# Performance work log

Hardware: AMD Instinct MI355X
Metric: run time of the kernel (lower is better)

## Reference

```python
import jax, jax.numpy as jnp
import numpy as np

B, T, D = 2, 2048, 2048
H, K, Hd = 16, 8, 128
EPS = 1e-6
THETA = 1e6


def _rms_norm(x, w):
    # x: [..., Hd]
    return x * jax.lax.rsqrt(jnp.mean(x * x, axis=-1, keepdims=True) + EPS) * w


def _rope(x, sin, cos):
    # x: [B, T, Hh, Hd]; sin/cos: [T, Hd//2]
    s = sin[None, :, None, :]
    c = cos[None, :, None, :]
    x1 = x[..., 0::2]
    x2 = x[..., 1::2]
    # NOTE: source concatenates halves (non-interleaved output), replicate exactly
    return jnp.concatenate([x1 * c - x2 * s, x1 * s + x2 * c], axis=-1)


def setup_inputs() -> dict:
    key = jax.random.key(0)
    ks = jax.random.split(key, 5)
    scale = 0.02
    x = jax.random.normal(ks[0], (B, T, D), dtype=jnp.float32)
    Wq = jax.random.normal(ks[1], (D, H * Hd), dtype=jnp.float32) * scale
    Wk = jax.random.normal(ks[2], (D, K * Hd), dtype=jnp.float32) * scale
    Wv = jax.random.normal(ks[3], (D, K * Hd), dtype=jnp.float32) * scale
    Wo = jax.random.normal(ks[4], (H * Hd, D), dtype=jnp.float32) * scale
    qn_w = jnp.ones((Hd,), dtype=jnp.float32)
    kn_w = jnp.ones((Hd,), dtype=jnp.float32)
    # RotaryEmbedding: inv_freq = theta**(-arange(0,Hd,2)/Hd); freqs = outer(t, inv_freq)
    inv_freq = 1.0 / (THETA ** (jnp.arange(0, Hd, 2, dtype=jnp.float32) / Hd))
    freqs = jnp.arange(T, dtype=jnp.float32)[:, None] * inv_freq[None, :]
    return {"x": x, "Wq": Wq, "Wk": Wk, "Wv": Wv, "Wo": Wo,
            "qn_w": qn_w, "kn_w": kn_w,
            "sin": jnp.sin(freqs), "cos": jnp.cos(freqs)}


def reference(x, Wq, Wk, Wv, Wo, qn_w, kn_w, sin, cos):
    Bx, Tx, _ = x.shape
    q = (x @ Wq).reshape(Bx, Tx, H, Hd)
    k = (x @ Wk).reshape(Bx, Tx, K, Hd)
    v = (x @ Wv).reshape(Bx, Tx, K, Hd)
    q = _rope(_rms_norm(q, qn_w), sin, cos)
    k = _rope(_rms_norm(k, kn_w), sin, cos)
    q = q.transpose(0, 2, 1, 3)  # [B,H,T,Hd]
    k = k.transpose(0, 2, 1, 3)  # [B,K,T,Hd]
    v = v.transpose(0, 2, 1, 3)
    if K != 1 and K != H:
        rep = H // K
        k = jnp.repeat(k, rep, axis=1)  # repeat_interleave on head dim
        v = jnp.repeat(v, rep, axis=1)
    att = jnp.einsum('bhqd,bhkd->bhqk', q.astype(jnp.float32),
                     k.astype(jnp.float32)) / np.sqrt(Hd).astype(np.float32)
    causal = jnp.tril(jnp.ones((Tx, Tx), dtype=bool))
    att = jnp.where(causal[None, None], att, -jnp.inf)
    att = jax.nn.softmax(att, axis=-1)
    out = jnp.einsum('bhqk,bhkd->bhqd', att, v.astype(jnp.float32))
    out = out.astype(q.dtype).transpose(0, 2, 1, 3).reshape(Bx, Tx, H * Hd)
    return out @ Wo
```

## Files before the change

kernel.cpp:

```cpp
#include <hip/hip_runtime.h>
#include <stdint.h>


#define B_ 2
#define T_ 2048
#define D_ 2048
#define H_ 16
#define KH_ 8
#define HD_ 128
#define M_ (B_*T_)
#define NQKV_ 4096
#define QK_SCALE_LOG2E 0.1275174337f

typedef unsigned short u16;
typedef unsigned int   u32;
typedef __attribute__((ext_vector_type(8)))  __bf16 bf16x8_t;
typedef __attribute__((ext_vector_type(4)))  float  f32x4_t;
typedef __attribute__((ext_vector_type(16))) float  f32x16_t;
typedef __attribute__((ext_vector_type(4)))  u32    u32x4_t;

__device__ __forceinline__ u16 f2bf(float f) {
    u32 x = __float_as_uint(f);
    return (u16)((x + 0x7fffu + ((x >> 16) & 1u)) >> 16);
}
__device__ __forceinline__ u32 pack2(u16 a, u16 b) { return (u32)a | ((u32)b << 16); }

__device__ __forceinline__ void gload16(const void* g, void* l) {
    __builtin_amdgcn_global_load_lds(
        (__attribute__((address_space(1))) const void*)(unsigned long long)g,
        (__attribute__((address_space(3))) void*)(u32)(unsigned long long)l,
        16, 0, 0);
}

__global__ void cast_x_kernel(const float* __restrict__ in, u16* __restrict__ out) {
    int i = (blockIdx.x * 256 + threadIdx.x) * 4;
    float4 v = *(const float4*)(in + i);
    u32 lo = pack2(f2bf(v.x), f2bf(v.y));
    u32 hi = pack2(f2bf(v.z), f2bf(v.w));
    *(uint2*)(out + i) = make_uint2(lo, hi);
}

__global__ void tcast_kernel(const float* __restrict__ in, u16* __restrict__ out,
                             int ncols) {
    __shared__ u16 tile[64][65];
    int k0 = blockIdx.x * 64;
    int n0 = blockIdx.y * 64;
    int tid = threadIdx.x;
#pragma unroll
    for (int i = 0; i < 8; ++i) {
        int idx = tid + i * 256;
        int r = idx >> 5, c2 = idx & 31;
        float2 v = *(const float2*)(in + (size_t)(k0 + r) * ncols + n0 + 2 * c2);
        tile[r][2 * c2]     = f2bf(v.x);
        tile[r][2 * c2 + 1] = f2bf(v.y);
    }
    __syncthreads();
#pragma unroll
    for (int i = 0; i < 8; ++i) {
        int idx = tid + i * 256;
        int rn = idx >> 5, c2 = idx & 31;
        *(u32*)(out + (size_t)(n0 + rn) * 2048 + k0 + 2 * c2) =
            pack2(tile[2 * c2][rn], tile[2 * c2 + 1][rn]);
    }
}

#define NKT 32

__global__ void __launch_bounds__(512, 2)
gemm8p_kernel(const u16* __restrict__ A, const u16* __restrict__ Bt,
              float* __restrict__ C, int N) {
    __shared__ u16 As[2][256 * 64];
    __shared__ u16 Bs[2][256 * 64];
    const int tid  = threadIdx.x;
    const int lane = tid & 63;
    const int w    = tid >> 6;
    const int wm   = w >> 2;
    const int wn   = w & 3;
    const int m0 = blockIdx.x * 256;
    const int n0 = blockIdx.y * 256;
    const int fr = lane & 15;
    const int kg = lane >> 4;

    const u16* Ag = A  + (size_t)m0 * 2048;
    const u16* Bg = Bt + (size_t)n0 * 2048;

#define STG(gbase, lbase, h, kt_)                                              \
    do {                                                                       \
        int _k0 = (kt_) * 64;                                                  \
        _Pragma("unroll")                                                      \
        for (int _i = 0; _i < 2; ++_i) {                                       \
            int _r  = _i * 64 + w * 8 + (lane >> 3);                           \
            int _sl = (lane & 7) ^ (_r & 7);                                   \
            gload16((gbase) + (size_t)((h) * 128 + _r) * 2048 + _k0 + _sl * 8, \
                    (lbase) + (h) * 8192 + (_i * 512 + w * 64) * 8);           \
        }                                                                      \
    } while (0)

    bf16x8_t afr[4][2];
    bf16x8_t bfr[2][2][2];
    f32x4_t  acc[8][4];
#pragma unroll
    for (int i = 0; i < 8; ++i)
#pragma unroll
        for (int j = 0; j < 4; ++j)
#pragma unroll
            for (int e = 0; e < 4; ++e) acc[i][j][e] = 0.0f;

#define RDA(qm)                                                                \
    _Pragma("unroll")                                                          \
    for (int _mf = 0; _mf < 4; ++_mf)                                          \
        _Pragma("unroll")                                                      \
        for (int _ks = 0; _ks < 2; ++_ks) {                                    \
            int _row  = wm * 128 + ((qm) * 4 + _mf) * 16 + fr;                 \
            int _phys = (_ks * 4 + kg) ^ (_row & 7);                           \
            afr[_mf][_ks] = *(const bf16x8_t*)(Asc + _row * 64 + _phys * 8);   \
        }
#define RDB(qn)                                                                \
    _Pragma("unroll")                                                          \
    for (int _nf = 0; _nf < 2; ++_nf)                                          \
        _Pragma("unroll")                                                      \
        for (int _ks = 0; _ks < 2; ++_ks) {                                    \
            int _row  = wn * 64 + ((qn) * 2 + _nf) * 16 + fr;                  \
            int _phys = (_ks * 4 + kg) ^ (_row & 7);                           \
            bfr[qn][_nf][_ks] = *(const bf16x8_t*)(Bsc + _row * 64 + _phys * 8);\
        }
#define MM(qm, qn)                                                             \
    _Pragma("unroll")                                                          \
    for (int _mf = 0; _mf < 4; ++_mf)                                          \
        _Pragma("unroll")                                                      \
        for (int _nf = 0; _nf < 2; ++_nf)                                      \
            _Pragma("unroll")                                                  \
            for (int _ks = 0; _ks < 2; ++_ks)                                  \
                acc[(qm) * 4 + _mf][(qn) * 2 + _nf] =                          \
                    __builtin_amdgcn_mfma_f32_16x16x32_bf16(                   \
                        afr[_mf][_ks], bfr[qn][_nf][_ks],                      \
                        acc[(qm) * 4 + _mf][(qn) * 2 + _nf], 0, 0, 0);

#define SBAR __builtin_amdgcn_sched_barrier(0)
#define PH_MID                                                                 \
    SBAR; __builtin_amdgcn_s_barrier();                                        \
    asm volatile("s_waitcnt lgkmcnt(0)" ::: "memory"); SBAR;                   \
    __builtin_amdgcn_s_setprio(1)
#define PH_END                                                                 \
    __builtin_amdgcn_s_setprio(0); SBAR;                                       \
    __builtin_amdgcn_s_barrier(); SBAR

    STG(Ag, &As[0][0], 0, 0);
    STG(Ag, &As[0][0], 1, 0);
    STG(Bg, &Bs[0][0], 0, 0);
    STG(Bg, &Bs[0][0], 1, 0);
    STG(Bg, &Bs[1][0], 0, 1);
    STG(Bg, &Bs[1][0], 1, 1);
    asm volatile("s_waitcnt vmcnt(4)" ::: "memory");
    SBAR;
    __builtin_amdgcn_s_barrier();
    SBAR;

    for (int kt = 0; kt < NKT; ++kt) {
        const int cur = kt & 1;
        const u16* Asc = &As[cur][0];
        const u16* Bsc = &Bs[cur][0];
        u16* Aso = &As[cur ^ 1][0];
        u16* Bsw = &Bs[cur][0];
        RDA(0); RDB(0);
        if (kt + 1 < NKT) STG(Ag, Aso, 0, kt + 1);
        PH_MID; MM(0, 0); PH_END;
        RDB(1);
        if (kt + 1 < NKT) STG(Ag, Aso, 1, kt + 1);
        PH_MID; MM(0, 1); PH_END;
        RDA(1);
        if (kt + 2 < NKT) STG(Bg, Bsw, 0, kt + 2);
        PH_MID; MM(1, 0); PH_END;
        if (kt + 2 < NKT) STG(Bg, Bsw, 1, kt + 2);
        SBAR; __builtin_amdgcn_s_barrier(); SBAR;
        __builtin_amdgcn_s_setprio(1);
        MM(1, 1);
        __builtin_amdgcn_s_setprio(0); SBAR;
        if (kt < NKT - 2) asm volatile("s_waitcnt vmcnt(4)" ::: "memory");
        else              asm volatile("s_waitcnt vmcnt(0)" ::: "memory");
        SBAR;
        __builtin_amdgcn_s_barrier();
        SBAR;
    }
#undef STG
#undef RDA
#undef RDB
#undef MM
#undef PH_MID
#undef PH_END

#pragma unroll
    for (int mf = 0; mf < 8; ++mf)
#pragma unroll
        for (int nf = 0; nf < 4; ++nf) {
            int colx  = n0 + wn * 64 + nf * 16 + fr;
            int rbase = m0 + wm * 128 + mf * 16 + kg * 4;
#pragma unroll
            for (int j = 0; j < 4; ++j)
                C[(size_t)(rbase + j) * N + colx] = acc[mf][nf][j];
        }
}

__global__ void __launch_bounds__(256)
normrope_kernel(const float* __restrict__ Cqkv,
                const float* __restrict__ qw, const float* __restrict__ kw,
                const float* __restrict__ sinT, const float* __restrict__ cosT,
                u16* __restrict__ qbf, u16* __restrict__ kbf, u16* __restrict__ vbf) {
    int lane = threadIdx.x & 63;
    int w    = threadIdx.x >> 6;
    int rid  = blockIdx.x * 4 + w;
    int m   = rid >> 5;
    int sub = rid & 31;
    int b = m >> 11, t = m & (T_ - 1);

    if (sub >= 24) {
        int kh = sub - 24;
        float2 x = *(const float2*)(Cqkv + (size_t)m * NQKV_ + 3072 + kh * HD_ + 2 * lane);
        *(u32*)(vbf + ((size_t)(b * KH_ + kh) * T_ + t) * HD_ + 2 * lane) =
            pack2(f2bf(x.x), f2bf(x.y));
        return;
    }
    bool isq = sub < 16;
    int  hh  = isq ? sub : sub - 16;
    int  colbase = isq ? hh * HD_ : 2048 + hh * HD_;
    float2 x = *(const float2*)(Cqkv + (size_t)m * NQKV_ + colbase + 2 * lane);
    float ss = x.x * x.x + x.y * x.y;
#pragma unroll
    for (int sh = 1; sh < 64; sh <<= 1) ss += __shfl_xor(ss, sh, 64);
    float scale = rsqrtf(ss * (1.0f / 128.0f) + 1e-6f);
    const float* wp = isq ? qw : kw;
    float2 wv = *(const float2*)(wp + 2 * lane);
    float y1 = x.x * scale * wv.x;
    float y2 = x.y * scale * wv.y;
    float c = cosT[t * 64 + lane], s = sinT[t * 64 + lane];
    float oa = y1 * c - y2 * s;
    float ob = y1 * s + y2 * c;
    if (isq) { oa *= QK_SCALE_LOG2E; ob *= QK_SCALE_LOG2E; }
    u16* outp = isq ? (qbf + ((size_t)(b * H_  + hh) * T_ + t) * HD_)
                    : (kbf + ((size_t)(b * KH_ + hh) * T_ + t) * HD_);
    outp[lane]      = f2bf(oa);
    outp[64 + lane] = f2bf(ob);
}

__global__ void vtrans_kernel(const u16* __restrict__ in, u16* __restrict__ out) {
    __shared__ u16 tile[64][65];
    int t0 = blockIdx.x * 64;
    int d0 = blockIdx.y * 64;
    size_t bi = (size_t)blockIdx.z * T_ * HD_;
    size_t bo = (size_t)blockIdx.z * HD_ * T_;
    int tid = threadIdx.x;
#pragma unroll
    for (int i = 0; i < 8; ++i) {
        int idx = tid + i * 256;
        int r = idx >> 5, c2 = idx & 31;
        u32 v = *(const u32*)(in + bi + (size_t)(t0 + r) * HD_ + d0 + 2 * c2);
        tile[r][2 * c2]     = (u16)(v & 0xffffu);
        tile[r][2 * c2 + 1] = (u16)(v >> 16);
    }
    __syncthreads();
#pragma unroll
    for (int i = 0; i < 8; ++i) {
        int idx = tid + i * 256;
        int rd = idx >> 5, c2 = idx & 31;
        *(u32*)(out + bo + (size_t)(d0 + rd) * T_ + t0 + 2 * c2) =
            pack2(tile[2 * c2][rd], tile[2 * c2 + 1][rd]);
    }
}

__global__ void __launch_bounds__(256, 2)
attn_kernel(const u16* __restrict__ qg, const u16* __restrict__ kgl,
            const u16* __restrict__ vtg, u16* __restrict__ attout) {
    __shared__ u16 Kt[2][64 * 128];
    __shared__ u16 Vt[2][128 * 64];

    const int tid = threadIdx.x, lane = tid & 63, w = tid >> 6;
    const int qb = (int)gridDim.x - 1 - (int)blockIdx.x;
    const int h = blockIdx.y, b = blockIdx.z;
    const int kh = h >> 1;
    const int q0 = qb * 128;
    const int col = lane & 31;
    const int hi  = lane >> 5;
    const int l7  = lane & 7;
    const int l15 = lane & 15;
    const int qw0 = q0 + w * 32;
    const int qlane = qw0 + col;

    const u16* qbase = qg  + ((size_t)(b * H_  + h ) * T_) * HD_;
    const u16* kbase = kgl + ((size_t)(b * KH_ + kh) * T_) * HD_;
    const u16* vbase = vtg + ((size_t)(b * KH_ + kh) * HD_) * T_;

    bf16x8_t qf[8];
#pragma unroll
    for (int s = 0; s < 8; ++s)
        qf[s] = *(const bf16x8_t*)(qbase + (size_t)qlane * HD_ + s * 16 + hi * 8);

    const int krl = lane >> 4, kcl = lane & 15;
    const int vrl = lane >> 3, vcl = lane & 7;

    f32x16_t o[4];
#pragma unroll
    for (int dt = 0; dt < 4; ++dt)
#pragma unroll
        for (int r = 0; r < 16; ++r) o[dt][r] = 0.0f;
    float mrow = -1e30f, lrow = 0.0f;

    const int nt = 2 * (qb + 1);

#define STAGE(buf, tt)                                                          \
    do {                                                                        \
        int kv0s = (tt) * 64;                                                   \
        _Pragma("unroll")                                                       \
        for (int cc = 0; cc < 4; ++cc) {                                        \
            int c = w * 4 + cc;                                                 \
            int r = c * 4 + krl;                                                \
            gload16(kbase + (size_t)(kv0s + r) * HD_ + (kcl ^ (r & 15)) * 8,    \
                    &Kt[buf][c * 512]);                                         \
            int rv = c * 8 + vrl;                                               \
            gload16(vbase + (size_t)rv * T_ + kv0s + (vcl ^ (rv & 7)) * 8,      \
                    &Vt[buf][c * 512]);                                         \
        }                                                                       \
    } while (0)

    STAGE(0, 0);
    __syncthreads();

    for (int t = 0; t < nt; ++t) {
        const int cur = t & 1;
        const int kv0 = t * 64;
        if (t + 1 < nt) STAGE(cur ^ 1, t + 1);

        if (kv0 <= qw0 + 31) {
            f32x16_t s0, s1;
#pragma unroll
            for (int r = 0; r < 16; ++r) { s0[r] = 0.0f; s1[r] = 0.0f; }
            __builtin_amdgcn_s_setprio(1);
#pragma unroll
            for (int ss = 0; ss < 8; ++ss) {
                bf16x8_t kf0 = *(const bf16x8_t*)
                    (&Kt[cur][col * 128 + (((2 * ss + hi) ^ l15) * 8)]);
                s0 = __builtin_amdgcn_mfma_f32_32x32x16_bf16(kf0, qf[ss], s0, 0, 0, 0);
                bf16x8_t kf1 = *(const bf16x8_t*)
                    (&Kt[cur][(32 + col) * 128 + (((2 * ss + hi) ^ l15) * 8)]);
                s1 = __builtin_amdgcn_mfma_f32_32x32x16_bf16(kf1, qf[ss], s1, 0, 0, 0);
            }
            __builtin_amdgcn_s_setprio(0);
            if (kv0 + 63 > qw0) {
#pragma unroll
                for (int r = 0; r < 16; ++r) {
                    int cr = (r & 3) + 8 * (r >> 2) + 4 * hi;
                    if (kv0 + cr      > qlane) s0[r] = -1e30f;
                    if (kv0 + 32 + cr > qlane) s1[r] = -1e30f;
                }
            }
            float tmax = s0[0];
#pragma unroll
            for (int r = 1; r < 16; ++r) tmax = fmaxf(tmax, s0[r]);
#pragma unroll
            for (int r = 0; r < 16; ++r) tmax = fmaxf(tmax, s1[r]);
            tmax = fmaxf(tmax, __shfl_xor(tmax, 32, 64));
            float mnew = fmaxf(mrow, tmax);
            float corr = exp2f(mrow - mnew);
            mrow = mnew;
            float ps = 0.0f;
#pragma unroll
            for (int r = 0; r < 16; ++r) {
                s0[r] = exp2f(s0[r] - mrow); ps += s0[r];
                s1[r] = exp2f(s1[r] - mrow); ps += s1[r];
            }
            lrow = lrow * corr + ps;
#pragma unroll
            for (int dt = 0; dt < 4; ++dt)
#pragma unroll
                for (int r = 0; r < 16; ++r) o[dt][r] *= corr;
            u32 pd0[8], pd1[8], po0[8], po1[8];
#pragma unroll
            for (int i = 0; i < 8; ++i) {
                pd0[i] = pack2(f2bf(s0[2 * i]), f2bf(s0[2 * i + 1]));
                pd1[i] = pack2(f2bf(s1[2 * i]), f2bf(s1[2 * i + 1]));
                po0[i] = __shfl_xor(pd0[i], 32, 64);
                po1[i] = __shfl_xor(pd1[i], 32, 64);
            }
            bf16x8_t pf[4];
#pragma unroll
            for (int ks = 0; ks < 4; ++ks) {
                const u32* pd = (ks < 2) ? pd0 : pd1;
                const u32* po = (ks < 2) ? po0 : po1;
                int base = (ks & 1) * 4;
                union { u32 u[4]; bf16x8_t v; } f;
                f.u[0] = hi ? po[base + 2] : pd[base + 0];
                f.u[1] = hi ? po[base + 3] : pd[base + 1];
                f.u[2] = hi ? pd[base + 2] : po[base + 0];
                f.u[3] = hi ? pd[base + 3] : po[base + 1];
                pf[ks] = f.v;
            }
            __builtin_amdgcn_s_setprio(1);
#pragma unroll
            for (int dt = 0; dt < 4; ++dt) {
                int dl = dt * 32 + col;
#pragma unroll
                for (int ks = 0; ks < 4; ++ks) {
                    bf16x8_t vf = *(const bf16x8_t*)
                        (&Vt[cur][dl * 64 + (((2 * ks + hi) ^ l7) * 8)]);
                    o[dt] = __builtin_amdgcn_mfma_f32_32x32x16_bf16(vf, pf[ks], o[dt], 0, 0, 0);
                }
            }
            __builtin_amdgcn_s_setprio(0);
        }
        __syncthreads();
    }
#undef STAGE

    float ltot = lrow + __shfl_xor(lrow, 32, 64);
    float inv  = 1.0f / ltot;
    u16* Tr = &Kt[0][0] + w * 4096;
#pragma unroll
    for (int dt = 0; dt < 4; ++dt)
#pragma unroll
        for (int g = 0; g < 4; ++g) {
            int slot = ((dt << 2) | g) ^ (col & 7);
            u32 lo  = pack2(f2bf(o[dt][4 * g + 0] * inv), f2bf(o[dt][4 * g + 1] * inv));
            u32 hi2 = pack2(f2bf(o[dt][4 * g + 2] * inv), f2bf(o[dt][4 * g + 3] * inv));
            *(uint2*)(Tr + col * 128 + slot * 8 + 4 * hi) = make_uint2(lo, hi2);
        }
    size_t rowbase = (size_t)(b * T_ + qw0);
#pragma unroll
    for (int p = 0; p < 8; ++p) {
        int ql   = p * 4 + (lane >> 4);
        int slot = lane & 15;
        int dl   = (slot ^ (ql & 7)) * 8;
        u32x4_t v = *(const u32x4_t*)(Tr + ql * 128 + slot * 8);
        *(u32x4_t*)(attout + (rowbase + ql) * 2048 + h * HD_ + dl) = v;
    }
}

extern "C" void kernel_launch(void* const* d_in, const int* in_sizes, int n_in,
                              void* d_out, int out_size, void* d_ws, size_t ws_size,
                              hipStream_t stream) {
    const float* x    = (const float*)d_in[0];
    const float* Wq   = (const float*)d_in[1];
    const float* Wk   = (const float*)d_in[2];
    const float* Wv   = (const float*)d_in[3];
    const float* Wo   = (const float*)d_in[4];
    const float* qw   = (const float*)d_in[5];
    const float* kw   = (const float*)d_in[6];
    const float* sinT = (const float*)d_in[7];
    const float* cosT = (const float*)d_in[8];
    float* out = (float*)d_out;

    u16*  x_bf   = (u16*)d_ws;
    u16*  wqkv_t = x_bf   + (size_t)M_ * D_;
    u16*  wo_t   = wqkv_t + (size_t)4096 * 2048;
    float* c_qkv = (float*)(wo_t + (size_t)2048 * 2048);
    u16*  q_bf   = (u16*)(c_qkv + (size_t)M_ * NQKV_);
    u16*  k_bf   = q_bf + (size_t)B_ * H_  * T_ * HD_;
    u16*  v_bf   = k_bf + (size_t)B_ * KH_ * T_ * HD_;
    u16*  v_t    = v_bf + (size_t)B_ * KH_ * T_ * HD_;
    u16*  att_bf = v_t  + (size_t)B_ * KH_ * T_ * HD_;

    cast_x_kernel<<<(M_ * D_) / 1024, 256, 0, stream>>>(x, x_bf);
    tcast_kernel<<<dim3(32, 32), 256, 0, stream>>>(Wq, wqkv_t, 2048);
    tcast_kernel<<<dim3(32, 16), 256, 0, stream>>>(Wk, wqkv_t + (size_t)2048 * 2048, 1024);
    tcast_kernel<<<dim3(32, 16), 256, 0, stream>>>(Wv, wqkv_t + (size_t)3072 * 2048, 1024);
    tcast_kernel<<<dim3(32, 32), 256, 0, stream>>>(Wo, wo_t, 2048);

    gemm8p_kernel<<<dim3(16, 16), 512, 0, stream>>>(x_bf, wqkv_t, c_qkv, 4096);
    normrope_kernel<<<(M_ * 32) / 4, 256, 0, stream>>>(c_qkv, qw, kw, sinT, cosT,
                                                       q_bf, k_bf, v_bf);
    vtrans_kernel<<<dim3(32, 2, 16), 256, 0, stream>>>(v_bf, v_t);
    attn_kernel<<<dim3(16, 16, 2), 256, 0, stream>>>(q_bf, k_bf, v_t, att_bf);
    gemm8p_kernel<<<dim3(16, 8), 512, 0, stream>>>(att_bf, wo_t, out, 2048);
}
```

Baseline: 397.3 us.

## Stage V through registers with single LDS buffer to raise attention occupancy

Result: slower. 578.6 us (+45.6%).

```diff
diff --git a/kernel.cpp b/kernel.cpp
--- a/kernel.cpp
+++ b/kernel.cpp
@@ -267,11 +267,11 @@
     }
 }
 
-__global__ void __launch_bounds__(256, 2)
+__global__ void __launch_bounds__(256, 3)
 attn_kernel(const u16* __restrict__ qg, const u16* __restrict__ kgl,
             const u16* __restrict__ vtg, u16* __restrict__ attout) {
     __shared__ u16 Kt[2][64 * 128];
-    __shared__ u16 Vt[2][128 * 64];
+    __shared__ u16 Vt[128 * 64];
 
     const int tid = threadIdx.x, lane = tid & 63, w = tid >> 6;
     const int qb = (int)gridDim.x - 1 - (int)blockIdx.x;
@@ -306,7 +306,11 @@
 
     const int nt = 2 * (qb + 1);
 
-#define STAGE(buf, tt)                                                          \
+    u32x4_t vrA[4], vrB[4];
+
+#define SBARR __builtin_amdgcn_sched_barrier(0)
+
+#define STAGE_K(buf, tt)                                                        \
     do {                                                                        \
         int kv0s = (tt) * 64;                                                   \
         _Pragma("unroll")                                                       \
@@ -315,100 +319,149 @@
             int r = c * 4 + krl;                                                \
             gload16(kbase + (size_t)(kv0s + r) * HD_ + (kcl ^ (r & 15)) * 8,    \
                     &Kt[buf][c * 512]);                                         \
-            int rv = c * 8 + vrl;                                               \
-            gload16(vbase + (size_t)rv * T_ + kv0s + (vcl ^ (rv & 7)) * 8,      \
-                    &Vt[buf][c * 512]);                                         \
         }                                                                       \
     } while (0)
 
-    STAGE(0, 0);
-    __syncthreads();
-
-    for (int t = 0; t < nt; ++t) {
-        const int cur = t & 1;
-        const int kv0 = t * 64;
-        if (t + 1 < nt) STAGE(cur ^ 1, t + 1);
-
-        if (kv0 <= qw0 + 31) {
-            f32x16_t s0, s1;
-#pragma unroll
-            for (int r = 0; r < 16; ++r) { s0[r] = 0.0f; s1[r] = 0.0f; }
-            __builtin_amdgcn_s_setprio(1);
-#pragma unroll
-            for (int ss = 0; ss < 8; ++ss) {
-                bf16x8_t kf0 = *(const bf16x8_t*)
-                    (&Kt[cur][col * 128 + (((2 * ss + hi) ^ l15) * 8)]);
-                s0 = __builtin_amdgcn_mfma_f32_32x32x16_bf16(kf0, qf[ss], s0, 0, 0, 0);
-                bf16x8_t kf1 = *(const bf16x8_t*)
-                    (&Kt[cur][(32 + col) * 128 + (((2 * ss + hi) ^ l15) * 8)]);
-                s1 = __builtin_amdgcn_mfma_f32_32x32x16_bf16(kf1, qf[ss], s1, 0, 0, 0);
-            }
-            __builtin_amdgcn_s_setprio(0);
-            if (kv0 + 63 > qw0) {
-#pragma unroll
-                for (int r = 0; r < 16; ++r) {
-                    int cr = (r & 3) + 8 * (r >> 2) + 4 * hi;
-                    if (kv0 + cr      > qlane) s0[r] = -1e30f;
-                    if (kv0 + 32 + cr > qlane) s1[r] = -1e30f;
-                }
-            }
-            float tmax = s0[0];
-#pragma unroll
-            for (int r = 1; r < 16; ++r) tmax = fmaxf(tmax, s0[r]);
-#pragma unroll
-            for (int r = 0; r < 16; ++r) tmax = fmaxf(tmax, s1[r]);
-            tmax = fmaxf(tmax, __shfl_xor(tmax, 32, 64));
-            float mnew = fmaxf(mrow, tmax);
-            float corr = exp2f(mrow - mnew);
-            mrow = mnew;
-            float ps = 0.0f;
-#pragma unroll
-            for (int r = 0; r < 16; ++r) {
-                s0[r] = exp2f(s0[r] - mrow); ps += s0[r];
-                s1[r] = exp2f(s1[r] - mrow); ps += s1[r];
-            }
-            lrow = lrow * corr + ps;
-#pragma unroll
-            for (int dt = 0; dt < 4; ++dt)
-#pragma unroll
-                for (int r = 0; r < 16; ++r) o[dt][r] *= corr;
-            u32 pd0[8], pd1[8], po0[8], po1[8];
-#pragma unroll
-            for (int i = 0; i < 8; ++i) {
-                pd0[i] = pack2(f2bf(s0[2 * i]), f2bf(s0[2 * i + 1]));
-                pd1[i] = pack2(f2bf(s1[2 * i]), f2bf(s1[2 * i + 1]));
-                po0[i] = __shfl_xor(pd0[i], 32, 64);
-                po1[i] = __shfl_xor(pd1[i], 32, 64);
-            }
-            bf16x8_t pf[4];
-#pragma unroll
-            for (int ks = 0; ks < 4; ++ks) {
-                const u32* pd = (ks < 2) ? pd0 : pd1;
-                const u32* po = (ks < 2) ? po0 : po1;
-                int base = (ks & 1) * 4;
-                union { u32 u[4]; bf16x8_t v; } f;
-                f.u[0] = hi ? po[base + 2] : pd[base + 0];
-                f.u[1] = hi ? po[base + 3] : pd[base + 1];
-                f.u[2] = hi ? pd[base + 2] : po[base + 0];
-                f.u[3] = hi ? pd[base + 3] : po[base + 1];
-                pf[ks] = f.v;
-            }
-            __builtin_amdgcn_s_setprio(1);
-#pragma unroll
-            for (int dt = 0; dt < 4; ++dt) {
-                int dl = dt * 32 + col;
-#pragma unroll
-                for (int ks = 0; ks < 4; ++ks) {
-                    bf16x8_t vf = *(const bf16x8_t*)
-                        (&Vt[cur][dl * 64 + (((2 * ks + hi) ^ l7) * 8)]);
-                    o[dt] = __builtin_amdgcn_mfma_f32_32x32x16_bf16(vf, pf[ks], o[dt], 0, 0, 0);
-                }
-            }
-            __builtin_amdgcn_s_setprio(0);
-        }
-        __syncthreads();
-    }
-#undef STAGE
+#define VLOAD(VR, tt)                                                           \
+    do {                                                                        \
+        int kv0s = (tt) * 64;                                                   \
+        _Pragma("unroll")                                                       \
+        for (int cc = 0; cc < 4; ++cc) {                                        \
+            int rv = (w * 4 + cc) * 8 + vrl;                                    \
+            VR[cc] = *(const u32x4_t*)(vbase + (size_t)rv * T_ + kv0s +         \
+                                       (vcl ^ (rv & 7)) * 8);                   \
+        }                                                                       \
+    } while (0)
+
+#define DSWR(VR)                                                                \
+    do {                                                                        \
+        _Pragma("unroll")                                                       \
+        for (int cc = 0; cc < 4; ++cc)                                          \
+            *(u32x4_t*)(Vt + (w * 4 + cc) * 512 + lane * 8) = VR[cc];           \
+    } while (0)
+
+#define COMPUTE(tt, CUR)                                                        \
+    do {                                                                        \
+        const int kv0 = (tt) * 64;                                              \
+        const bool act = (kv0 <= qw0 + 31);                                     \
+        f32x16_t s0, s1;                                                        \
+        bf16x8_t pf[4];                                                         \
+        if (act) {                                                              \
+            _Pragma("unroll")                                                   \
+            for (int r = 0; r < 16; ++r) { s0[r] = 0.0f; s1[r] = 0.0f; }        \
+            __builtin_amdgcn_s_setprio(1);                                      \
+            _Pragma("unroll")                                                   \
+            for (int ss = 0; ss < 8; ++ss) {                                    \
+                bf16x8_t kf0 = *(const bf16x8_t*)                               \
+                    (&Kt[CUR][col * 128 + (((2 * ss + hi) ^ l15) * 8)]);        \
+                s0 = __builtin_amdgcn_mfma_f32_32x32x16_bf16(kf0, qf[ss], s0, 0, 0, 0); \
+                bf16x8_t kf1 = *(const bf16x8_t*)                               \
+                    (&Kt[CUR][(32 + col) * 128 + (((2 * ss + hi) ^ l15) * 8)]); \
+                s1 = __builtin_amdgcn_mfma_f32_32x32x16_bf16(kf1, qf[ss], s1, 0, 0, 0); \
+            }                                                                   \
+            __builtin_amdgcn_s_setprio(0);                                      \
+            if (kv0 + 63 > qw0) {                                               \
+                _Pragma("unroll")                                               \
+                for (int r = 0; r < 16; ++r) {                                  \
+                    int cr = (r & 3) + 8 * (r >> 2) + 4 * hi;                   \
+                    if (kv0 + cr      > qlane) s0[r] = -1e30f;                  \
+                    if (kv0 + 32 + cr > qlane) s1[r] = -1e30f;                  \
+                }                                                               \
+            }                                                                   \
+            float tmax = s0[0];                                                 \
+            _Pragma("unroll")                                                   \
+            for (int r = 1; r < 16; ++r) tmax = fmaxf(tmax, s0[r]);             \
+            _Pragma("unroll")                                                   \
+            for (int r = 0; r < 16; ++r) tmax = fmaxf(tmax, s1[r]);             \
+            tmax = fmaxf(tmax, __shfl_xor(tmax, 32, 64));                       \
+            float mnew = fmaxf(mrow, tmax);                                     \
+            float corr = exp2f(mrow - mnew);                                    \
+            mrow = mnew;                                                        \
+            float ps = 0.0f;                                                    \
+            _Pragma("unroll")                                                   \
+            for (int r = 0; r < 16; ++r) {                                      \
+                s0[r] = exp2f(s0[r] - mrow); ps += s0[r];                       \
+                s1[r] = exp2f(s1[r] - mrow); ps += s1[r];                       \
+            }                                                                   \
+            lrow = lrow * corr + ps;                                            \
+            _Pragma("unroll")                                                   \
+            for (int dt = 0; dt < 4; ++dt)                                      \
+                _Pragma("unroll")                                               \
+                for (int r = 0; r < 16; ++r) o[dt][r] *= corr;                  \
+            u32 pd0[8], pd1[8], po0[8], po1[8];                                 \
+            _Pragma("unroll")                                                   \
+            for (int i = 0; i < 8; ++i) {                                       \
+                pd0[i] = pack2(f2bf(s0[2 * i]), f2bf(s0[2 * i + 1]));           \
+                pd1[i] = pack2(f2bf(s1[2 * i]), f2bf(s1[2 * i + 1]));           \
+                po0[i] = __shfl_xor(pd0[i], 32, 64);                            \
+                po1[i] = __shfl_xor(pd1[i], 32, 64);                            \
+            }                                                                   \
+            _Pragma("unroll")                                                   \
+            for (int ks = 0; ks < 4; ++ks) {                                    \
+                const u32* pd = (ks < 2) ? pd0 : pd1;                           \
+                const u32* po = (ks < 2) ? po0 : po1;                           \
+                int base = (ks & 1) * 4;                                        \
+                union { u32 u[4]; bf16x8_t v; } f;                              \
+                f.u[0] = hi ? po[base + 2] : pd[base + 0];                      \
+                f.u[1] = hi ? po[base + 3] : pd[base + 1];                      \
+                f.u[2] = hi ? pd[base + 2] : po[base + 0];                      \
+                f.u[3] = hi ? pd[base + 3] : po[base + 1];                      \
+                pf[ks] = f.v;                                                   \
+            }                                                                   \
+        }                                                                       \
+                                         \
+        asm volatile("s_waitcnt lgkmcnt(0)" ::: "memory");                      \
+        SBARR;                                                                  \
+        __builtin_amdgcn_s_barrier();                                           \
+        SBARR;                                                                  \
+        if (act) {                                                              \
+            __builtin_amdgcn_s_setprio(1);                                      \
+            _Pragma("unroll")                                                   \
+            for (int dt = 0; dt < 4; ++dt) {                                    \
+                int dl = dt * 32 + col;                                         \
+                _Pragma("unroll")                                               \
+                for (int ks = 0; ks < 4; ++ks) {                                \
+                    bf16x8_t vf = *(const bf16x8_t*)                            \
+                        (&Vt[dl * 64 + (((2 * ks + hi) ^ l7) * 8)]);            \
+                    o[dt] = __builtin_amdgcn_mfma_f32_32x32x16_bf16(vf, pf[ks], o[dt], 0, 0, 0); \
+                }                                                               \
+            }                                                                   \
+            __builtin_amdgcn_s_setprio(0);                                      \
+        }                                                                       \
+    } while (0)
+
+#define TILE(tt, CUR, VC, VN)                                                   \
+    do {                                                                        \
+        asm volatile("s_waitcnt vmcnt(0)" ::: "memory");                        \
+        SBARR;                                                                  \
+        DSWR(VC);                                                               \
+        if ((tt) + 1 < nt) { STAGE_K((CUR) ^ 1, (tt) + 1); VLOAD(VN, (tt) + 1); } \
+        COMPUTE(tt, CUR);                                                       \
+        SBARR;                                                                  \
+        if ((tt) + 1 < nt) asm volatile("s_waitcnt vmcnt(4)" ::: "memory");     \
+        else               asm volatile("s_waitcnt vmcnt(0)" ::: "memory");     \
+        SBARR;                                                                  \
+        __builtin_amdgcn_s_barrier();                                           \
+        SBARR;                                                                  \
+    } while (0)
+
+    STAGE_K(0, 0);
+    VLOAD(vrA, 0);
+    asm volatile("s_waitcnt vmcnt(4)" ::: "memory");
+    SBARR;
+    __builtin_amdgcn_s_barrier();
+    SBARR;
+
+    for (int it = 0; it < nt; it += 2) {
+        TILE(it,     0, vrA, vrB);
+        TILE(it + 1, 1, vrB, vrA);
+    }
+#undef TILE
+#undef COMPUTE
+#undef DSWR
+#undef VLOAD
+#undef STAGE_K
+#undef SBARR
 
     float ltot = lrow + __shfl_xor(lrow, 32, 64);
     float inv  = 1.0f / ltot;
```
